# Kernel optimization log

Measured on AMD Instinct MI355X. Metric: run time of the kernel, lower is better.

Reference implementation:

```python
import jax, jax.numpy as jnp
import numpy as np

HEAD_DIM = 64
SELECT = 256  # number of selected rows/cols (m)
NUM_ITER = 4  # Newton-Schulz iterations


def _select_idx(T, mask, m):
    # top-k over sum of features (select_type='sum'), done under stop_gradient (torch.no_grad)
    somme = jax.lax.stop_gradient(jnp.sum(T, axis=-1))  # [B,H,N]
    neg = -jnp.finfo(somme.dtype).max
    somme = jnp.where(mask[:, None, :], somme, neg)
    _, idx = jax.lax.top_k(somme, m)  # [B,H,m], descending like argsort(descending=True)[:m]
    return idx


def _gather_rows(T, idx):
    # T: [B,H,N,D], idx: [B,H,m] -> [B,H,m,D]  (index_select over flattened (b h n))
    return jnp.take_along_axis(T, idx[..., None], axis=2)


def _iterative_inv(mat, num_iter):
    m = mat.shape[-1]
    I = jnp.eye(m, dtype=mat.dtype)
    K = mat
    # V0 = K^T / max_j(sum_i K_ij)
    scale = 1.0 / jnp.max(jnp.sum(K, axis=-2), axis=-1)[:, :, None, None]
    V = scale * jnp.swapaxes(K, -1, -2)
    for _ in range(num_iter):
        KV = jnp.matmul(K, V)
        V = jnp.matmul(0.25 * V, 13.0 * I - jnp.matmul(KV, 15.0 * I - jnp.matmul(KV, 7.0 * I - KV)))
    return V


def setup_inputs() -> dict:
    key = jax.random.key(0)
    kq, kk, kv = jax.random.split(key, 3)
    B, H, N, D = 2, 8, 4096, HEAD_DIM
    Q = jax.random.normal(kq, (B, H, N, D), dtype=jnp.float32)
    K = jax.random.normal(kk, (B, H, N, D), dtype=jnp.float32)
    V = jax.random.normal(kv, (B, H, N, D), dtype=jnp.float32)
    mask = jnp.ones((B, N), dtype=bool)
    return {"Q": Q, "K": K, "V": V, "mask": mask}


def reference(Q, K, V, mask):
    m = SELECT
    Qs = Q / np.sqrt(HEAD_DIM).astype(np.float32)
    # select_mode='default' -> index_select_different: indices for K from K, for Q from (scaled) Q
    idx_k = _select_idx(K, mask, m)
    idx_q = _select_idx(Qs, mask, m)
    nc = _gather_rows(K, idx_k)   # [B,H,m,D] selected columns (from K)
    nr = _gather_rows(Qs, idx_k := idx_q if False else idx_q) if False else _gather_rows(Qs, idx_q)  # [B,H,m,D]
    c = jnp.einsum('bhnd,bhmd->bhnm', Qs, nc)   # [B,H,N,m]
    r = jnp.einsum('bhmd,bhnd->bhmn', nr, K)    # [B,H,m,N]
    neg = -jnp.finfo(Qs.dtype).max
    r = jnp.where(mask[:, None, None, :], r, neg)
    kernel_1 = jax.nn.softmax(c, axis=-1)                 # [B,H,N,m]
    u = _gather_rows(kernel_1, idx_q)                     # [B,H,m,m]
    kernel_3 = jax.nn.softmax(r, axis=-1)                 # [B,H,m,N]
    kernel_2_inv = _iterative_inv(u, NUM_ITER)            # [B,H,m,m]
    RV = jnp.matmul(kernel_3, V)                          # [B,H,m,D]
    X = jnp.matmul(kernel_1, jnp.matmul(kernel_2_inv, RV))  # [B,H,N,D]
    return X
```

## Files before the change

### kernel.cpp

```cpp
#include <hip/hip_runtime.h>
#include <float.h>


#define G    16
#define NSEQ 4096
#define DH   64
#define MSEL 256
#define NSL  16

typedef __attribute__((ext_vector_type(8))) short short8;
typedef __attribute__((ext_vector_type(4))) float floatx4;
typedef __attribute__((ext_vector_type(4))) unsigned short ushort4v;
typedef unsigned short ush;

static __device__ __forceinline__ ush f2b(float x) {
    union { float f; unsigned u; } c{x};
    unsigned r = c.u + 0x7FFFu + ((c.u >> 16) & 1u);
    return (ush)(r >> 16);
}
static __device__ __forceinline__ float b2f(ush h) {
    union { unsigned u; float f; } c{(unsigned)h << 16};
    return c.f;
}
static __device__ __forceinline__ void split_store(ush* __restrict__ h, ush* __restrict__ l,
                                                   int off, float4 v, float scale) {
    float a0 = v.x * scale, a1 = v.y * scale, a2 = v.z * scale, a3 = v.w * scale;
    ush h0 = f2b(a0), h1 = f2b(a1), h2 = f2b(a2), h3 = f2b(a3);
    ushort4v hv = { h0, h1, h2, h3 };
    ushort4v lv = { f2b(a0 - b2f(h0)), f2b(a1 - b2f(h1)), f2b(a2 - b2f(h2)), f2b(a3 - b2f(h3)) };
    *(ushort4v*)&h[off] = hv;
    *(ushort4v*)&l[off] = lv;
}
static __device__ __forceinline__ floatx4 mfma3(short8 ah, short8 al, short8 bh, short8 bl, floatx4 acc) {
    acc = __builtin_amdgcn_mfma_f32_16x16x32_bf16(al, bh, acc, 0, 0, 0);
    acc = __builtin_amdgcn_mfma_f32_16x16x32_bf16(ah, bl, acc, 0, 0, 0);
    acc = __builtin_amdgcn_mfma_f32_16x16x32_bf16(ah, bh, acc, 0, 0, 0);
    return acc;
}

__global__ __launch_bounds__(256) void rowsum_kernel(const float* __restrict__ Q, const float* __restrict__ K,
                                                     float* __restrict__ sumQ, float* __restrict__ sumK,
                                                     float* __restrict__ k2) {
    long row = (long)blockIdx.x * 16 + (threadIdx.x >> 4);
    int c4 = (threadIdx.x & 15) * 4;
    float4 q = *(const float4*)(Q + row * DH + c4);
    float4 k = *(const float4*)(K + row * DH + c4);
    float qs = q.x + q.y + q.z + q.w;
    float ks = k.x + k.y + k.z + k.w;
    float k2s = k.x * k.x + k.y * k.y + k.z * k.z + k.w * k.w;
#pragma unroll
    for (int off = 8; off; off >>= 1) {
        qs += __shfl_xor(qs, off); ks += __shfl_xor(ks, off); k2s += __shfl_xor(k2s, off);
    }
    if ((threadIdx.x & 15) == 0) { sumQ[row] = qs; sumK[row] = ks; k2[row] = k2s; }
}

__global__ __launch_bounds__(256) void topk_select(const float* __restrict__ sumQ, const float* __restrict__ sumK,
                                                   int* __restrict__ idxQ, int* __restrict__ idxK,
                                                   const float* __restrict__ k2, float* __restrict__ Kmax2,
                                                   float* __restrict__ colsum) {
    __shared__ unsigned red[4];
    __shared__ float redf[4];
    __shared__ unsigned eqpre[64];
    __shared__ unsigned cnt_sel;
    int g = blockIdx.x, which = blockIdx.y;
    const float* s = (which ? sumK : sumQ) + (long)g * NSEQ;
    int* out = (which ? idxK : idxQ) + g * MSEL;
    int t = threadIdx.x, lane = t & 63, wid = t >> 6;
    if (which == 0) colsum[g * 256 + t] = 0.f;
    unsigned k[16];
#pragma unroll
    for (int i = 0; i < 16; i++) {
        unsigned u = __float_as_uint(s[t + 256 * i]);
        k[i] = (u & 0x80000000u) ? ~u : (u | 0x80000000u);
    }
    unsigned T = 0;
    for (int b = 31; b >= 0; b--) {
        unsigned trial = T | (1u << b);
        int c = 0;
#pragma unroll
        for (int i = 0; i < 16; i++) c += (k[i] >= trial);
#pragma unroll
        for (int off = 32; off; off >>= 1) c += __shfl_xor(c, off);
        __syncthreads();
        if (lane == 0) red[wid] = (unsigned)c;
        __syncthreads();
        unsigned tot = red[0] + red[1] + red[2] + red[3];
        if (tot == MSEL) { T = trial; break; }
        if (tot > MSEL) T = trial;
    }
    int cg = 0;
#pragma unroll
    for (int i = 0; i < 16; i++) cg += (k[i] > T);
#pragma unroll
    for (int off = 32; off; off >>= 1) cg += __shfl_xor(cg, off);
    __syncthreads();
    if (lane == 0) red[wid] = (unsigned)cg;
    if (t == 0) cnt_sel = 0;
    __syncthreads();
    unsigned ngreater = red[0] + red[1] + red[2] + red[3];
    unsigned want_eq = MSEL - ngreater;
#pragma unroll
    for (int i = 0; i < 16; i++) {
        unsigned long long be = __ballot(k[i] == T);
        if (lane == 0) eqpre[i * 4 + wid] = (unsigned)__popcll(be);
    }
    __syncthreads();
    if (t == 0) {
        unsigned run = 0;
        for (int j = 0; j < 64; j++) { unsigned c = eqpre[j]; eqpre[j] = run; run += c; }
    }
    __syncthreads();
#pragma unroll
    for (int i = 0; i < 16; i++) {
        int idx = t + 256 * i;
        unsigned long long lt = (1ull << lane) - 1;
        bool gt = (k[i] > T);
        unsigned long long bg = __ballot(gt);
        unsigned wbase = 0;
        if (lane == 0) wbase = atomicAdd(&cnt_sel, (unsigned)__popcll(bg));
        wbase = __shfl((int)wbase, 0);
        if (gt) out[wbase + __popcll(bg & lt)] = idx;
        bool eq = (k[i] == T);
        unsigned long long be = __ballot(eq);
        if (eq) {
            unsigned rank = eqpre[i * 4 + wid] + (unsigned)__popcll(be & lt);
            if (rank < want_eq) out[ngreater + rank] = idx;
        }
    }
    if (which == 1) {
        float mx = 0.f;
#pragma unroll
        for (int i = 0; i < 16; i++) mx = fmaxf(mx, k2[(long)g * NSEQ + t + 256 * i]);
#pragma unroll
        for (int off = 32; off; off >>= 1) mx = fmaxf(mx, __shfl_xor(mx, off));
        __syncthreads();
        if (lane == 0) redf[wid] = mx;
        __syncthreads();
        if (t == 0) Kmax2[g] = fmaxf(fmaxf(redf[0], redf[1]), fmaxf(redf[2], redf[3]));
    }
}

__global__ __launch_bounds__(256) void gather_kernel(const float* __restrict__ Q, const float* __restrict__ K,
                                                     const int* __restrict__ idxQ, const int* __restrict__ idxK,
                                                     const float* __restrict__ Kmax2,
                                                     float* __restrict__ nr,
                                                     ush* __restrict__ ncH, ush* __restrict__ ncL,
                                                     float* __restrict__ Mb) {
    int wid = threadIdx.x >> 6, lane = threadIdx.x & 63;
    long t = (long)blockIdx.x * 4 + wid;
    long g = t >> 8;
    int iq = idxQ[t], ik = idxK[t];
    float qv = Q[(g * NSEQ + iq) * DH + lane] * 0.125f;
    nr[t * DH + lane] = qv;
    float kv = K[(g * NSEQ + ik) * DH + lane];
    ush h = f2b(kv);
    ncH[t * DH + lane] = h;
    ncL[t * DH + lane] = f2b(kv - b2f(h));
    float n2 = qv * qv;
#pragma unroll
    for (int off = 32; off; off >>= 1) n2 += __shfl_xor(n2, off);
    if (lane == 0) Mb[t] = sqrtf(n2 * Kmax2[g]);
}

__global__ __launch_bounds__(256, 4) void flash_rv(const float* __restrict__ nr, const float* __restrict__ K,
                                                   const float* __restrict__ V, const float* __restrict__ Mb,
                                                   float* __restrict__ Lp, float* __restrict__ RVp) {
    __shared__ __align__(16) ush B1h[64 * 72];
    __shared__ __align__(16) ush B1l[64 * 72];
    __shared__ __align__(16) ush Ph[64 * 72];
    __shared__ float msh[64];
    __shared__ float lred[64][2];
    int ns = blockIdx.x, s = blockIdx.y, g = blockIdx.z;
    int t = threadIdx.x, lane = t & 63, w = t >> 6;
    int wr = w >> 1, wc = w & 1, ml = lane & 15, quad = lane >> 4;
    int lr = t >> 2, lq = t & 3;
    const float* nrg = nr + (long)g * 16384 + (long)s * 64 * 64;
    const float* Kg  = K + (long)g * 262144 + (long)ns * 256 * 64;
    const float* Vg  = V + (long)g * 262144 + (long)ns * 256 * 64;
    short8 Ah[2][2], Al[2][2];
#pragma unroll
    for (int i2 = 0; i2 < 2; i2++)
#pragma unroll
        for (int kq = 0; kq < 2; kq++) {
            const float* p = nrg + (wr * 32 + i2 * 16 + ml) * 64 + kq * 32 + quad * 8;
            float4 f0 = *(const float4*)p;
            float4 f1 = *(const float4*)(p + 4);
            float vals[8] = { f0.x, f0.y, f0.z, f0.w, f1.x, f1.y, f1.z, f1.w };
            short8 hh, ll;
#pragma unroll
            for (int j = 0; j < 8; j++) {
                ush h = f2b(vals[j]);
                hh[j] = (short)h;
                ll[j] = (short)f2b(vals[j] - b2f(h));
            }
            Ah[i2][kq] = hh; Al[i2][kq] = ll;
        }
    if (t < 64) msh[t] = Mb[g * 256 + s * 64 + t];
    float lsum[2][4] = {};
    floatx4 acc[2][2] = {};
    int vn = t >> 2, vdq = (t & 3) * 16;
    for (int it = 0; it < 4; it++) {
        __syncthreads();
        float4 kv[4], vv[4];
#pragma unroll
        for (int q = 0; q < 4; q++) kv[q] = *(const float4*)(Kg + (long)(it * 64 + lr) * 64 + lq * 16 + q * 4);
#pragma unroll
        for (int q = 0; q < 4; q++) vv[q] = *(const float4*)(Vg + (long)(it * 64 + vn) * 64 + vdq + q * 4);
#pragma unroll
        for (int q = 0; q < 4; q++) split_store(B1h, B1l, lr * 72 + lq * 16 + q * 4, kv[q], 1.0f);
        __syncthreads();
        floatx4 sa[2][2] = {};
#pragma unroll
        for (int kq = 0; kq < 2; kq++) {
            short8 b0h = *(const short8*)&B1h[(wc * 32 + ml) * 72 + kq * 32 + quad * 8];
            short8 b0l = *(const short8*)&B1l[(wc * 32 + ml) * 72 + kq * 32 + quad * 8];
            short8 b1h = *(const short8*)&B1h[(wc * 32 + 16 + ml) * 72 + kq * 32 + quad * 8];
            short8 b1l = *(const short8*)&B1l[(wc * 32 + 16 + ml) * 72 + kq * 32 + quad * 8];
            sa[0][0] = mfma3(Ah[0][kq], Al[0][kq], b0h, b0l, sa[0][0]);
            sa[0][1] = mfma3(Ah[0][kq], Al[0][kq], b1h, b1l, sa[0][1]);
            sa[1][0] = mfma3(Ah[1][kq], Al[1][kq], b0h, b0l, sa[1][0]);
            sa[1][1] = mfma3(Ah[1][kq], Al[1][kq], b1h, b1l, sa[1][1]);
        }
        __syncthreads();
#pragma unroll
        for (int i2 = 0; i2 < 2; i2++)
#pragma unroll
            for (int r = 0; r < 4; r++) {
                int row = wr * 32 + i2 * 16 + quad * 4 + r;
                float M = msh[row];
                float p0 = __expf(sa[i2][0][r] - M);
                float p1 = __expf(sa[i2][1][r] - M);
                lsum[i2][r] += p0 + p1;
                Ph[row * 72 + wc * 32 + ml] = f2b(p0);
                Ph[row * 72 + wc * 32 + 16 + ml] = f2b(p1);
            }
#pragma unroll
        for (int q = 0; q < 4; q++)
#pragma unroll
            for (int c = 0; c < 4; c++) {
                int d = vdq + q * 4 + c;
                int addr = d * 72 + ((((vn >> 3) ^ ((d >> 4) & 3)) << 3) | (vn & 7));
                B1h[addr] = f2b((&vv[q].x)[c]);
            }
        __syncthreads();
#pragma unroll
        for (int kq = 0; kq < 2; kq++) {
            short8 a0 = *(const short8*)&Ph[(wr * 32 + ml) * 72 + kq * 32 + quad * 8];
            short8 a1 = *(const short8*)&Ph[(wr * 32 + 16 + ml) * 72 + kq * 32 + quad * 8];
            int nb = kq * 4 + quad;
            short8 b0 = *(const short8*)&B1h[(wc * 32 + ml) * 72 + ((nb ^ (2 * wc)) << 3)];
            short8 b1 = *(const short8*)&B1h[(wc * 32 + 16 + ml) * 72 + ((nb ^ (2 * wc + 1)) << 3)];
            acc[0][0] = __builtin_amdgcn_mfma_f32_16x16x32_bf16(a0, b0, acc[0][0], 0, 0, 0);
            acc[0][1] = __builtin_amdgcn_mfma_f32_16x16x32_bf16(a0, b1, acc[0][1], 0, 0, 0);
            acc[1][0] = __builtin_amdgcn_mfma_f32_16x16x32_bf16(a1, b0, acc[1][0], 0, 0, 0);
            acc[1][1] = __builtin_amdgcn_mfma_f32_16x16x32_bf16(a1, b1, acc[1][1], 0, 0, 0);
        }
    }
#pragma unroll
    for (int i2 = 0; i2 < 2; i2++)
#pragma unroll
        for (int r = 0; r < 4; r++) {
            float v = lsum[i2][r];
#pragma unroll
            for (int off = 8; off; off >>= 1) v += __shfl_xor(v, off);
            if (ml == 0) lred[wr * 32 + i2 * 16 + quad * 4 + r][wc] = v;
        }
    __syncthreads();
    long p = ((long)(g * 4 + s)) * NSL + ns;
    if (t < 64) Lp[p * 64 + t] = lred[t][0] + lred[t][1];
    float* rvp = RVp + p * 4096;
#pragma unroll
    for (int i2 = 0; i2 < 2; i2++)
#pragma unroll
        for (int j2 = 0; j2 < 2; j2++)
#pragma unroll
            for (int r = 0; r < 4; r++)
                rvp[(wr * 32 + i2 * 16 + quad * 4 + r) * 64 + wc * 32 + j2 * 16 + ml] = acc[i2][j2][r];
}

__global__ __launch_bounds__(256) void rv_merge(const float* __restrict__ Lp, const float* __restrict__ RVp,
                                                ush* __restrict__ RVt) {
    int g = blockIdx.y;
    int s = blockIdx.x >> 2, mq = blockIdx.x & 3;
    int t = threadIdx.x;
    int d = t & 63;
    int m0 = mq * 16 + (t >> 6) * 4;
    long pb = ((long)(g * 4 + s)) * NSL;
#pragma unroll
    for (int mm = 0; mm < 4; mm++) {
        int rho = m0 + mm;
        float L = 0.f, val = 0.f;
#pragma unroll
        for (int n = 0; n < NSL; n++) {
            L   += Lp[(pb + n) * 64 + rho];
            val += RVp[(pb + n) * 4096 + rho * 64 + d];
        }
        RVt[(long)g * 16384 + d * 256 + s * 64 + rho] = f2b(val / L);
    }
}

template <int MODE>
__global__ __launch_bounds__(256, 4) void fused_cx(const float* __restrict__ A,
                                                   const ush* __restrict__ ncH, const ush* __restrict__ ncL,
                                                   const ush* __restrict__ WtH, const ush* __restrict__ WtL,
                                                   float* __restrict__ Out, float* __restrict__ colsum,
                                                   float ascale) {
    __shared__ __align__(16) ush SM[18432];
    ush* Ah = SM;            ush* Al = SM + 4608;
    ush* Bh = SM + 9216;     ush* Bl = SM + 13824;
    ush* Ph = SM;            ush* Pl = SM + 4608;
    ush* Wh = SM + 9216;     ush* Wl = SM + 13824;
    __shared__ float pm[256], ps[256], Mr[64], Lr[64];
    int strip = blockIdx.x, g = blockIdx.y;
    int t = threadIdx.x, lane = t & 63, w = t >> 6;
    int wr = w >> 1, wc = w & 1, ml = lane & 15, quad = lane >> 4;
    int lr = t >> 2, lq = t & 3;
    long aRows = (MODE == 0) ? 4096 : 256;
    const float* Ag = A + (long)g * aRows * 64 + (long)strip * 64 * 64;
    const ush* ncHg = ncH + (long)g * 16384;
    const ush* ncLg = ncL + (long)g * 16384;
#pragma unroll
    for (int q = 0; q < 4; q++) {
        float4 v = *(const float4*)(Ag + lr * 64 + lq * 16 + q * 4);
        split_store(Ah, Al, lr * 72 + lq * 16 + q * 4, v, ascale);
    }
    floatx4 sacc[4][4] = {};
    for (int c = 0; c < 4; c++) {
        __syncthreads();
        {
            const ush* sH = ncHg + (c * 64 + lr) * 64;
            const ush* sL = ncLg + (c * 64 + lr) * 64;
            *(uint4*)&Bh[lr * 72 + lq * 8]       = *(const uint4*)&sH[lq * 8];
            *(uint4*)&Bh[lr * 72 + (lq + 4) * 8] = *(const uint4*)&sH[(lq + 4) * 8];
            *(uint4*)&Bl[lr * 72 + lq * 8]       = *(const uint4*)&sL[lq * 8];
            *(uint4*)&Bl[lr * 72 + (lq + 4) * 8] = *(const uint4*)&sL[(lq + 4) * 8];
        }
        __syncthreads();
#pragma unroll
        for (int kq = 0; kq < 2; kq++) {
            short8 bh = *(const short8*)&Bh[(w * 16 + ml) * 72 + kq * 32 + quad * 8];
            short8 bl = *(const short8*)&Bl[(w * 16 + ml) * 72 + kq * 32 + quad * 8];
#pragma unroll
            for (int i = 0; i < 4; i++) {
                short8 afh = *(const short8*)&Ah[(16 * i + ml) * 72 + kq * 32 + quad * 8];
                short8 afl = *(const short8*)&Al[(16 * i + ml) * 72 + kq * 32 + quad * 8];
                sacc[c][i] = mfma3(afh, afl, bh, bl, sacc[c][i]);
            }
        }
    }
#pragma unroll
    for (int i = 0; i < 4; i++)
#pragma unroll
        for (int r = 0; r < 4; r++) {
            float mx = fmaxf(fmaxf(sacc[0][i][r], sacc[1][i][r]), fmaxf(sacc[2][i][r], sacc[3][i][r]));
#pragma unroll
            for (int off = 8; off; off >>= 1) mx = fmaxf(mx, __shfl_xor(mx, off));
            if (ml == 0) pm[(16 * i + quad * 4 + r) * 4 + w] = mx;
        }
    __syncthreads();
    if (t < 64) Mr[t] = fmaxf(fmaxf(pm[t * 4], pm[t * 4 + 1]), fmaxf(pm[t * 4 + 2], pm[t * 4 + 3]));
    __syncthreads();
#pragma unroll
    for (int i = 0; i < 4; i++)
#pragma unroll
        for (int r = 0; r < 4; r++) {
            int row = 16 * i + quad * 4 + r;
            float M = Mr[row];
            float sum = 0.f;
#pragma unroll
            for (int c = 0; c < 4; c++) {
                float p = __expf(sacc[c][i][r] - M);
                sacc[c][i][r] = p;
                sum += p;
            }
#pragma unroll
            for (int off = 8; off; off >>= 1) sum += __shfl_xor(sum, off);
            if (ml == 0) ps[row * 4 + w] = sum;
        }
    __syncthreads();
    if (t < 64) Lr[t] = ps[t * 4] + ps[t * 4 + 1] + ps[t * 4 + 2] + ps[t * 4 + 3];
    __syncthreads();
    if (MODE == 1) {
        float invL[4][4];
#pragma unroll
        for (int i = 0; i < 4; i++)
#pragma unroll
            for (int r = 0; r < 4; r++) invL[i][r] = 1.0f / Lr[16 * i + quad * 4 + r];
        float* ug = Out + (long)g * 65536 + (long)strip * 64 * 256;
#pragma unroll
        for (int i = 0; i < 4; i++)
#pragma unroll
            for (int r = 0; r < 4; r++) {
                int row = 16 * i + quad * 4 + r;
#pragma unroll
                for (int c = 0; c < 4; c++)
                    ug[(long)row * 256 + c * 64 + w * 16 + ml] = sacc[c][i][r] * invL[i][r];
            }
#pragma unroll
        for (int c = 0; c < 4; c++) {
            float v = 0.f;
#pragma unroll
            for (int i = 0; i < 4; i++)
#pragma unroll
                for (int r = 0; r < 4; r++) v += sacc[c][i][r] * invL[i][r];
            v += __shfl_xor(v, 16);
            v += __shfl_xor(v, 32);
            if (quad == 0) atomicAdd(&colsum[g * 256 + c * 64 + w * 16 + ml], v);
        }
        return;
    }
    floatx4 xacc[2][2] = {};
    const ush* wHg = WtH + (long)g * 16384;
    const ush* wLg = WtL + (long)g * 16384;
#pragma unroll
    for (int h = 0; h < 4; h++) {
        __syncthreads();
#pragma unroll
        for (int i = 0; i < 4; i++)
#pragma unroll
            for (int r = 0; r < 4; r++) {
                int row = 16 * i + quad * 4 + r;
                float p = sacc[h][i][r];
                ush hh = f2b(p);
                Ph[row * 72 + w * 16 + ml] = hh;
                Pl[row * 72 + w * 16 + ml] = f2b(p - b2f(hh));
            }
        {
            const ush* sH = wHg + lr * 256 + h * 64;
            const ush* sL = wLg + lr * 256 + h * 64;
            *(uint4*)&Wh[lr * 72 + lq * 8]       = *(const uint4*)&sH[lq * 8];
            *(uint4*)&Wh[lr * 72 + (lq + 4) * 8] = *(const uint4*)&sH[(lq + 4) * 8];
            *(uint4*)&Wl[lr * 72 + lq * 8]       = *(const uint4*)&sL[lq * 8];
            *(uint4*)&Wl[lr * 72 + (lq + 4) * 8] = *(const uint4*)&sL[(lq + 4) * 8];
        }
        __syncthreads();
#pragma unroll
        for (int kq = 0; kq < 2; kq++) {
            short8 a0h = *(const short8*)&Ph[(wr * 32 + ml) * 72 + kq * 32 + quad * 8];
            short8 a0l = *(const short8*)&Pl[(wr * 32 + ml) * 72 + kq * 32 + quad * 8];
            short8 a1h = *(const short8*)&Ph[(wr * 32 + 16 + ml) * 72 + kq * 32 + quad * 8];
            short8 a1l = *(const short8*)&Pl[(wr * 32 + 16 + ml) * 72 + kq * 32 + quad * 8];
            short8 b0h = *(const short8*)&Wh[(wc * 32 + ml) * 72 + kq * 32 + quad * 8];
            short8 b0l = *(const short8*)&Wl[(wc * 32 + ml) * 72 + kq * 32 + quad * 8];
            short8 b1h = *(const short8*)&Wh[(wc * 32 + 16 + ml) * 72 + kq * 32 + quad * 8];
            short8 b1l = *(const short8*)&Wl[(wc * 32 + 16 + ml) * 72 + kq * 32 + quad * 8];
            xacc[0][0] = mfma3(a0h, a0l, b0h, b0l, xacc[0][0]);
            xacc[0][1] = mfma3(a0h, a0l, b1h, b1l, xacc[0][1]);
            xacc[1][0] = mfma3(a1h, a1l, b0h, b0l, xacc[1][0]);
            xacc[1][1] = mfma3(a1h, a1l, b1h, b1l, xacc[1][1]);
        }
    }
    float* outg = Out + (long)g * 262144 + (long)strip * 64 * 64;
#pragma unroll
    for (int i2 = 0; i2 < 2; i2++)
#pragma unroll
        for (int j2 = 0; j2 < 2; j2++)
#pragma unroll
            for (int r = 0; r < 4; r++) {
                int row = wr * 32 + i2 * 16 + quad * 4 + r;
                outg[(long)row * 64 + wc * 32 + j2 * 16 + ml] = xacc[i2][j2][r] / Lr[row];
            }
}

__global__ __launch_bounds__(256) void ns_prep_kernel(const float* __restrict__ u, const float* __restrict__ colsum,
                                                      ush* __restrict__ u_bf, ush* __restrict__ V0,
                                                      float* __restrict__ scale) {
    __shared__ float tile[64][65];
    __shared__ float smax[4];
    int g = blockIdx.z, tr = blockIdx.y, tc = blockIdx.x;
    int t = threadIdx.x, lane = t & 63, wid = t >> 6;
    float v = colsum[g * 256 + t];
#pragma unroll
    for (int off = 32; off; off >>= 1) v = fmaxf(v, __shfl_xor(v, off));
    if (lane == 0) smax[wid] = v;
    __syncthreads();
    float sc = 1.0f / fmaxf(fmaxf(smax[0], smax[1]), fmaxf(smax[2], smax[3]));
    if (t == 0 && tr == 0 && tc == 0) scale[g] = sc;
    long base = (long)g * MSEL * MSEL;
    const float* ug = u + base;
    int cq = (t & 15) * 4, r0 = t >> 4;
#pragma unroll
    for (int i = 0; i < 4; i++) {
        int r = r0 + 16 * i;
        float4 vv = *(const float4*)&ug[(long)(tr * 64 + r) * MSEL + tc * 64 + cq];
        long o = base + (long)(tr * 64 + r) * MSEL + tc * 64 + cq;
        ushort4v ub = { f2b(vv.x), f2b(vv.y), f2b(vv.z), f2b(vv.w) };
        *(ushort4v*)&u_bf[o] = ub;
        tile[r][cq] = vv.x; tile[r][cq + 1] = vv.y; tile[r][cq + 2] = vv.z; tile[r][cq + 3] = vv.w;
    }
    __syncthreads();
#pragma unroll
    for (int i = 0; i < 4; i++) {
        int r = r0 + 16 * i;
        ushort4v o = { f2b(sc * tile[cq][r]), f2b(sc * tile[cq + 1][r]),
                       f2b(sc * tile[cq + 2][r]), f2b(sc * tile[cq + 3][r]) };
        *(ushort4v*)&V0[base + (long)(tc * 64 + r) * MSEL + tr * 64 + cq] = o;
    }
}

template <int MODE>
__global__ __launch_bounds__(256) void ns2(const ush* __restrict__ A0, const ush* __restrict__ A1,
                                           const ush* __restrict__ Bt,
                                           ush* __restrict__ O0rm, ush* __restrict__ O0t,
                                           ush* __restrict__ O1rm, ush* __restrict__ O1t,
                                           const ush* __restrict__ Et_in, const ush* __restrict__ St_in,
                                           const float* __restrict__ scale) {
    const int LD = 136;
    __shared__ __align__(16) ush As[64 * LD];
    __shared__ __align__(16) ush Bs[64 * LD];
    int z = blockIdx.z, g = z & 15, which = z >> 4;
    int tm = blockIdx.y, tn = blockIdx.x;
    long base = (long)g * 65536;
    const ush* A = which ? A1 : A0;
    ush* Orm = which ? O1rm : O0rm;
    ush* Ot  = which ? O1t  : O0t;
    const ush* Ag = A + base + (long)tm * 64 * 256;
    long bbase = (MODE >= 3) ? (long)g * 16384 : base;
    const ush* Bg = Bt + bbase + (long)tn * 64 * 256;
    int t = threadIdx.x;
    int lr = t >> 2, lq = t & 3;
    int w = t >> 6, lane = t & 63;
    int wr = w >> 1, wc = w & 1;
    int ml = lane & 15, quad = lane >> 4;
    floatx4 acc[2][2] = {};
#pragma unroll
    for (int h = 0; h < 2; h++) {
        __syncthreads();
#pragma unroll
        for (int rr = 0; rr < 4; rr++) {
            int col = (lq + 4 * rr) * 8;
            *(uint4*)&As[lr * LD + col] = *(const uint4*)(Ag + lr * 256 + h * 128 + col);
            *(uint4*)&Bs[lr * LD + col] = *(const uint4*)(Bg + lr * 256 + h * 128 + col);
        }
        __syncthreads();
#pragma unroll
        for (int kq = 0; kq < 4; kq++) {
            int ko = kq * 32 + quad * 8;
            short8 a0 = *(const short8*)&As[(wr * 32 + ml) * LD + ko];
            short8 a1 = *(const short8*)&As[(wr * 32 + 16 + ml) * LD + ko];
            short8 b0 = *(const short8*)&Bs[(wc * 32 + ml) * LD + ko];
            short8 b1 = *(const short8*)&Bs[(wc * 32 + 16 + ml) * LD + ko];
            acc[0][0] = __builtin_amdgcn_mfma_f32_16x16x32_bf16(a0, b0, acc[0][0], 0, 0, 0);
            acc[0][1] = __builtin_amdgcn_mfma_f32_16x16x32_bf16(a0, b1, acc[0][1], 0, 0, 0);
            acc[1][0] = __builtin_amdgcn_mfma_f32_16x16x32_bf16(a1, b0, acc[1][0], 0, 0, 0);
            acc[1][1] = __builtin_amdgcn_mfma_f32_16x16x32_bf16(a1, b1, acc[1][1], 0, 0, 0);
        }
    }
    float sc = (MODE == 1) ? scale[g] : 1.0f;
    int rowb = tm * 64 + wr * 32, colb = tn * 64 + wc * 32;
#pragma unroll
    for (int i = 0; i < 2; i++) {
#pragma unroll
        for (int j = 0; j < 2; j++) {
            int col = colb + j * 16 + ml;
            int r0 = rowb + i * 16 + quad * 4;
            float v[4];
#pragma unroll
            for (int r = 0; r < 4; r++) v[r] = acc[i][j][r];
            if (MODE == 1) {
#pragma unroll
                for (int r = 0; r < 4; r++) v[r] *= sc;
            } else if (MODE == 2) {
                ushort4v et = *(const ushort4v*)&Et_in[base + (long)col * 256 + r0];
                ushort4v st = *(const ushort4v*)&St_in[base + (long)col * 256 + r0];
#pragma unroll
                for (int r = 0; r < 4; r++)
                    v[r] = 0.25f * (((r0 + r == col) ? 13.0f : 0.0f)
                                    - 15.0f * b2f(et[r]) + 7.0f * b2f(st[r]) - v[r]);
            }
            if (MODE == 3) {
                ushort4v ht = { f2b(v[0]), f2b(v[1]), f2b(v[2]), f2b(v[3]) };
                *(ushort4v*)&Ot[(long)g * 16384 + (long)col * 256 + r0] = ht;
            } else if (MODE == 4) {
                ushort4v hv, lv;
#pragma unroll
                for (int r = 0; r < 4; r++) {
                    ush h = f2b(v[r]);
                    hv[r] = h;
                    lv[r] = f2b(v[r] - b2f(h));
                }
                *(ushort4v*)&O0rm[(long)g * 16384 + (long)col * 256 + r0] = hv;
                *(ushort4v*)&O0t[(long)g * 16384 + (long)col * 256 + r0] = lv;
            } else {
                ush h[4];
#pragma unroll
                for (int r = 0; r < 4; r++) h[r] = f2b(v[r]);
#pragma unroll
                for (int r = 0; r < 4; r++) Orm[base + (long)(r0 + r) * 256 + col] = h[r];
                ushort4v ht = { h[0], h[1], h[2], h[3] };
                *(ushort4v*)&Ot[base + (long)col * 256 + r0] = ht;
            }
        }
    }
}

extern "C" void kernel_launch(void* const* d_in, const int* in_sizes, int n_in,
                              void* d_out, int out_size, void* d_ws, size_t ws_size,
                              hipStream_t stream) {
    (void)in_sizes; (void)n_in; (void)out_size; (void)ws_size;
    const float* Q = (const float*)d_in[0];
    const float* K = (const float*)d_in[1];
    const float* V = (const float*)d_in[2];

    float* ws    = (float*)d_ws;
    float* sumQ  = ws;
    float* sumK  = sumQ + 65536;
    float* k2    = sumK + 65536;
    float* nr    = k2 + 65536;
    float* u     = nr + 262144;
    float* Mb    = u + 1048576;
    float* Kmax2 = Mb + 4096;
    float* scale = Kmax2 + 16;
    float* colsum= scale + 16 + 32;
    float* Lp    = colsum + 4096;
    float* RVp   = Lp + 65536;
    int* idxQ    = (int*)(RVp + 4194304);
    int* idxK    = idxQ + 4096;
    ush* ncH     = (ush*)(idxK + 4096);
    ush* ncL     = ncH + 262144;
    ush* WtH     = ncL + 262144;
    ush* WtL     = WtH + 262144;
    ush* RVt     = WtL + 262144;
    ush* PRt     = RVt + 262144;
    ush* u_bf    = PRt + 262144;
    ush* Vacc_a  = u_bf + 1048576;
    ush* Vacc_b  = Vacc_a + 1048576;
    ush* VaccTj  = Vacc_b + 1048576;
    ush* E_a     = VaccTj + 1048576;
    ush* Et_a    = E_a + 1048576;
    ush* E_b     = Et_a + 1048576;
    ush* Et_b    = E_b + 1048576;
    ush* Sbuf    = Et_b + 1048576;
    ush* St      = Sbuf + 1048576;
    ush* Pbuf    = St + 1048576;
    ush* Pt      = Pbuf + 1048576;

    dim3 blk(256);

    hipLaunchKernelGGL(rowsum_kernel, dim3(G * NSEQ / 16), blk, 0, stream, Q, K, sumQ, sumK, k2);
    hipLaunchKernelGGL(topk_select, dim3(G, 2), blk, 0, stream, sumQ, sumK, idxQ, idxK, k2, Kmax2, colsum);
    hipLaunchKernelGGL(gather_kernel, dim3(G * MSEL / 4), blk, 0, stream, Q, K, idxQ, idxK, Kmax2, nr, ncH, ncL, Mb);

    hipLaunchKernelGGL(flash_rv, dim3(NSL, 4, G), blk, 0, stream, nr, K, V, Mb, Lp, RVp);
    hipLaunchKernelGGL(rv_merge, dim3(16, G), blk, 0, stream, Lp, RVp, RVt);

    hipLaunchKernelGGL((fused_cx<1>), dim3(4, G), blk, 0, stream, nr, ncH, ncL,
                       (const ush*)0, (const ush*)0, u, colsum, 1.0f);

    hipLaunchKernelGGL(ns_prep_kernel, dim3(4, 4, G), blk, 0, stream, u, colsum, u_bf, Vacc_a, scale);

    hipLaunchKernelGGL((ns2<1>), dim3(4, 4, G), blk, 0, stream,
                       u_bf, (const ush*)0, u_bf, E_a, Et_a, (ush*)0, (ush*)0,
                       (const ush*)0, (const ush*)0, scale);

    ush* E = E_a;  ush* Et = Et_a;
    ush* En = E_b; ush* Ent = Et_b;
    ush* Vc = Vacc_a; ush* Vn = Vacc_b;
    for (int i = 0; i < 4; i++) {
        hipLaunchKernelGGL((ns2<0>), dim3(4, 4, G), blk, 0, stream,
                           E, (const ush*)0, Et, Sbuf, St, (ush*)0, (ush*)0,
                           (const ush*)0, (const ush*)0, (const float*)0);
        hipLaunchKernelGGL((ns2<2>), dim3(4, 4, G), blk, 0, stream,
                           Sbuf, (const ush*)0, Et, Pbuf, Pt, (ush*)0, (ush*)0,
                           Et, St, (const float*)0);
        if (i < 3) {
            hipLaunchKernelGGL((ns2<0>), dim3(4, 4, 2 * G), blk, 0, stream,
                               E, Vc, Pt, En, Ent, Vn, VaccTj,
                               (const ush*)0, (const ush*)0, (const float*)0);
            ush* tp;
            tp = E; E = En; En = tp;
            tp = Et; Et = Ent; Ent = tp;
            tp = Vc; Vc = Vn; Vn = tp;
        }
    }
    hipLaunchKernelGGL((ns2<3>), dim3(1, 4, G), blk, 0, stream,
                       Pbuf, (const ush*)0, RVt, (ush*)0, PRt, (ush*)0, (ush*)0,
                       (const ush*)0, (const ush*)0, (const float*)0);
    hipLaunchKernelGGL((ns2<4>), dim3(1, 4, G), blk, 0, stream,
                       Vc, (const ush*)0, PRt, WtH, WtL, (ush*)0, (ush*)0,
                       (const ush*)0, (const ush*)0, (const float*)0);

    hipLaunchKernelGGL((fused_cx<0>), dim3(64, G), blk, 0, stream, Q, ncH, ncL, WtH, WtL,
                       (float*)d_out, (float*)0, 0.125f);
}
```

Measured before the change: 262.4 us.

## Restructure Newton-Schulz inverse chain into fused dual-GEMM steps and merge prep kernels

Rewrites the iterative inverse schedule. The next E = K·V is computed algebraically inside the step kernel from E, S=E², and E³, so the separate E² GEMM per iteration disappears. Each nsB block now computes two products, E³ and E⁴, and writes both P and the next E. The final P·RV ordering becomes V·P then (·RV), and rv_merge is folded into the ns prep kernel, which cuts launches. The risk is extra bf16 error accumulation, because E is now derived from polynomial terms instead of a direct product.

```diff
diff --git a/kernel.cpp b/kernel.cpp
--- a/kernel.cpp
+++ b/kernel.cpp
@@ -277,27 +277,6 @@
 #pragma unroll
             for (int r = 0; r < 4; r++)
                 rvp[(wr * 32 + i2 * 16 + quad * 4 + r) * 64 + wc * 32 + j2 * 16 + ml] = acc[i2][j2][r];
-}
-
-__global__ __launch_bounds__(256) void rv_merge(const float* __restrict__ Lp, const float* __restrict__ RVp,
-                                                ush* __restrict__ RVt) {
-    int g = blockIdx.y;
-    int s = blockIdx.x >> 2, mq = blockIdx.x & 3;
-    int t = threadIdx.x;
-    int d = t & 63;
-    int m0 = mq * 16 + (t >> 6) * 4;
-    long pb = ((long)(g * 4 + s)) * NSL;
-#pragma unroll
-    for (int mm = 0; mm < 4; mm++) {
-        int rho = m0 + mm;
-        float L = 0.f, val = 0.f;
-#pragma unroll
-        for (int n = 0; n < NSL; n++) {
-            L   += Lp[(pb + n) * 64 + rho];
-            val += RVp[(pb + n) * 4096 + rho * 64 + d];
-        }
-        RVt[(long)g * 16384 + d * 256 + s * 64 + rho] = f2b(val / L);
-    }
 }
 
 template <int MODE>
@@ -463,13 +442,34 @@
             }
 }
 
-__global__ __launch_bounds__(256) void ns_prep_kernel(const float* __restrict__ u, const float* __restrict__ colsum,
-                                                      ush* __restrict__ u_bf, ush* __restrict__ V0,
-                                                      float* __restrict__ scale) {
+__global__ __launch_bounds__(256) void mergeprep_kernel(const float* __restrict__ Lp, const float* __restrict__ RVp,
+                                                        ush* __restrict__ RVt,
+                                                        const float* __restrict__ u, const float* __restrict__ colsum,
+                                                        ush* __restrict__ u_bf, ush* __restrict__ V0,
+                                                        float* __restrict__ scale) {
     __shared__ float tile[64][65];
     __shared__ float smax[4];
-    int g = blockIdx.z, tr = blockIdx.y, tc = blockIdx.x;
+    int g = blockIdx.y;
     int t = threadIdx.x, lane = t & 63, wid = t >> 6;
+    if (blockIdx.z == 0) {
+        int s = blockIdx.x >> 2, mq = blockIdx.x & 3;
+        int d = t & 63;
+        int m0 = mq * 16 + (t >> 6) * 4;
+        long pb = ((long)(g * 4 + s)) * NSL;
+#pragma unroll
+        for (int mm = 0; mm < 4; mm++) {
+            int rho = m0 + mm;
+            float L = 0.f, val = 0.f;
+#pragma unroll
+            for (int n = 0; n < NSL; n++) {
+                L   += Lp[(pb + n) * 64 + rho];
+                val += RVp[(pb + n) * 4096 + rho * 64 + d];
+            }
+            RVt[(long)g * 16384 + d * 256 + s * 64 + rho] = f2b(val / L);
+        }
+        return;
+    }
+    int tc = blockIdx.x & 3, tr = (blockIdx.x >> 2) & 3;
     float v = colsum[g * 256 + t];
 #pragma unroll
     for (int off = 32; off; off >>= 1) v = fmaxf(v, __shfl_xor(v, off));
@@ -499,25 +499,19 @@
     }
 }
 
-template <int MODE>
-__global__ __launch_bounds__(256) void ns2(const ush* __restrict__ A0, const ush* __restrict__ A1,
-                                           const ush* __restrict__ Bt,
-                                           ush* __restrict__ O0rm, ush* __restrict__ O0t,
-                                           ush* __restrict__ O1rm, ush* __restrict__ O1t,
-                                           const ush* __restrict__ Et_in, const ush* __restrict__ St_in,
-                                           const float* __restrict__ scale) {
+__global__ __launch_bounds__(256) void nsAC(const ush* __restrict__ A0, const ush* __restrict__ B0t,
+                                            const ush* __restrict__ A1, const ush* __restrict__ B1t,
+                                            ush* __restrict__ C0rm, ush* __restrict__ C0t,
+                                            ush* __restrict__ C1rm,
+                                            const float* __restrict__ scale, int whichBase) {
     const int LD = 136;
     __shared__ __align__(16) ush As[64 * LD];
     __shared__ __align__(16) ush Bs[64 * LD];
-    int z = blockIdx.z, g = z & 15, which = z >> 4;
+    int z = blockIdx.z, g = z & 15, which = (z >> 4) + whichBase;
     int tm = blockIdx.y, tn = blockIdx.x;
     long base = (long)g * 65536;
-    const ush* A = which ? A1 : A0;
-    ush* Orm = which ? O1rm : O0rm;
-    ush* Ot  = which ? O1t  : O0t;
-    const ush* Ag = A + base + (long)tm * 64 * 256;
-    long bbase = (MODE >= 3) ? (long)g * 16384 : base;
-    const ush* Bg = Bt + bbase + (long)tn * 64 * 256;
+    const ush* Ag = (which ? A1 : A0) + base + (long)tm * 64 * 256;
+    const ush* Bg = (which ? B1t : B0t) + base + (long)tn * 64 * 256;
     int t = threadIdx.x;
     int lr = t >> 2, lq = t & 3;
     int w = t >> 6, lane = t & 63;
@@ -547,7 +541,7 @@
             acc[1][1] = __builtin_amdgcn_mfma_f32_16x16x32_bf16(a1, b1, acc[1][1], 0, 0, 0);
         }
     }
-    float sc = (MODE == 1) ? scale[g] : 1.0f;
+    float sc = (which == 0 && scale) ? scale[g] : 1.0f;
     int rowb = tm * 64 + wr * 32, colb = tn * 64 + wc * 32;
 #pragma unroll
     for (int i = 0; i < 2; i++) {
@@ -555,42 +549,164 @@
         for (int j = 0; j < 2; j++) {
             int col = colb + j * 16 + ml;
             int r0 = rowb + i * 16 + quad * 4;
-            float v[4];
-#pragma unroll
-            for (int r = 0; r < 4; r++) v[r] = acc[i][j][r];
-            if (MODE == 1) {
-#pragma unroll
-                for (int r = 0; r < 4; r++) v[r] *= sc;
-            } else if (MODE == 2) {
-                ushort4v et = *(const ushort4v*)&Et_in[base + (long)col * 256 + r0];
-                ushort4v st = *(const ushort4v*)&St_in[base + (long)col * 256 + r0];
-#pragma unroll
-                for (int r = 0; r < 4; r++)
-                    v[r] = 0.25f * (((r0 + r == col) ? 13.0f : 0.0f)
-                                    - 15.0f * b2f(et[r]) + 7.0f * b2f(st[r]) - v[r]);
-            }
-            if (MODE == 3) {
-                ushort4v ht = { f2b(v[0]), f2b(v[1]), f2b(v[2]), f2b(v[3]) };
-                *(ushort4v*)&Ot[(long)g * 16384 + (long)col * 256 + r0] = ht;
-            } else if (MODE == 4) {
-                ushort4v hv, lv;
+            ush h[4];
+#pragma unroll
+            for (int r = 0; r < 4; r++) h[r] = f2b(acc[i][j][r] * sc);
+            if (which == 0) {
+#pragma unroll
+                for (int r = 0; r < 4; r++) C0rm[base + (long)(r0 + r) * 256 + col] = h[r];
+                ushort4v ht = { h[0], h[1], h[2], h[3] };
+                *(ushort4v*)&C0t[base + (long)col * 256 + r0] = ht;
+            } else {
+#pragma unroll
+                for (int r = 0; r < 4; r++) C1rm[base + (long)(r0 + r) * 256 + col] = h[r];
+            }
+        }
+    }
+}
+
+template <bool FINAL>
+__global__ __launch_bounds__(256) void nsB(const ush* __restrict__ S, const ush* __restrict__ Et,
+                                           const ush* __restrict__ St,
+                                           ush* __restrict__ Eo, ush* __restrict__ Eot,
+                                           ush* __restrict__ Pt) {
+    const int LD = 136;
+    __shared__ __align__(16) ush As[64 * LD];
+    __shared__ __align__(16) ush B1s[64 * LD];
+    __shared__ __align__(16) ush B2s[64 * LD];
+    int g = blockIdx.z, tm = blockIdx.y, tn = blockIdx.x;
+    long base = (long)g * 65536;
+    const ush* Ag  = S + base + (long)tm * 64 * 256;
+    const ush* B1g = Et + base + (long)tn * 64 * 256;
+    const ush* B2g = St + base + (long)tn * 64 * 256;
+    int t = threadIdx.x;
+    int lr = t >> 2, lq = t & 3;
+    int w = t >> 6, lane = t & 63;
+    int wr = w >> 1, wc = w & 1;
+    int ml = lane & 15, quad = lane >> 4;
+    floatx4 acc1[2][2] = {};
+    floatx4 acc2[2][2] = {};
+#pragma unroll
+    for (int h = 0; h < 2; h++) {
+        __syncthreads();
+#pragma unroll
+        for (int rr = 0; rr < 4; rr++) {
+            int col = (lq + 4 * rr) * 8;
+            *(uint4*)&As[lr * LD + col]  = *(const uint4*)(Ag + lr * 256 + h * 128 + col);
+            *(uint4*)&B1s[lr * LD + col] = *(const uint4*)(B1g + lr * 256 + h * 128 + col);
+            if (!FINAL) *(uint4*)&B2s[lr * LD + col] = *(const uint4*)(B2g + lr * 256 + h * 128 + col);
+        }
+        __syncthreads();
+#pragma unroll
+        for (int kq = 0; kq < 4; kq++) {
+            int ko = kq * 32 + quad * 8;
+            short8 a0 = *(const short8*)&As[(wr * 32 + ml) * LD + ko];
+            short8 a1 = *(const short8*)&As[(wr * 32 + 16 + ml) * LD + ko];
+            short8 b10 = *(const short8*)&B1s[(wc * 32 + ml) * LD + ko];
+            short8 b11 = *(const short8*)&B1s[(wc * 32 + 16 + ml) * LD + ko];
+            acc1[0][0] = __builtin_amdgcn_mfma_f32_16x16x32_bf16(a0, b10, acc1[0][0], 0, 0, 0);
+            acc1[0][1] = __builtin_amdgcn_mfma_f32_16x16x32_bf16(a0, b11, acc1[0][1], 0, 0, 0);
+            acc1[1][0] = __builtin_amdgcn_mfma_f32_16x16x32_bf16(a1, b10, acc1[1][0], 0, 0, 0);
+            acc1[1][1] = __builtin_amdgcn_mfma_f32_16x16x32_bf16(a1, b11, acc1[1][1], 0, 0, 0);
+            if (!FINAL) {
+                short8 b20 = *(const short8*)&B2s[(wc * 32 + ml) * LD + ko];
+                short8 b21 = *(const short8*)&B2s[(wc * 32 + 16 + ml) * LD + ko];
+                acc2[0][0] = __builtin_amdgcn_mfma_f32_16x16x32_bf16(a0, b20, acc2[0][0], 0, 0, 0);
+                acc2[0][1] = __builtin_amdgcn_mfma_f32_16x16x32_bf16(a0, b21, acc2[0][1], 0, 0, 0);
+                acc2[1][0] = __builtin_amdgcn_mfma_f32_16x16x32_bf16(a1, b20, acc2[1][0], 0, 0, 0);
+                acc2[1][1] = __builtin_amdgcn_mfma_f32_16x16x32_bf16(a1, b21, acc2[1][1], 0, 0, 0);
+            }
+        }
+    }
+    int rowb = tm * 64 + wr * 32, colb = tn * 64 + wc * 32;
+#pragma unroll
+    for (int i = 0; i < 2; i++) {
+#pragma unroll
+        for (int j = 0; j < 2; j++) {
+            int col = colb + j * 16 + ml;
+            int r0 = rowb + i * 16 + quad * 4;
+            ushort4v et = *(const ushort4v*)&Et[base + (long)col * 256 + r0];
+            ushort4v st = *(const ushort4v*)&St[base + (long)col * 256 + r0];
+            ushort4v pv;
+#pragma unroll
+            for (int r = 0; r < 4; r++) {
+                float e = b2f(et[r]), s = b2f(st[r]);
+                float p = 0.25f * (((r0 + r == col) ? 13.0f : 0.0f) - 15.0f * e + 7.0f * s - acc1[i][j][r]);
+                pv[r] = f2b(p);
+            }
+            *(ushort4v*)&Pt[base + (long)col * 256 + r0] = pv;
+            if (!FINAL) {
+                ush h[4];
 #pragma unroll
                 for (int r = 0; r < 4; r++) {
-                    ush h = f2b(v[r]);
-                    hv[r] = h;
-                    lv[r] = f2b(v[r] - b2f(h));
+                    float e = b2f(et[r]), s = b2f(st[r]);
+                    float en = 0.25f * (13.0f * e - 15.0f * s + 7.0f * acc1[i][j][r] - acc2[i][j][r]);
+                    h[r] = f2b(en);
                 }
-                *(ushort4v*)&O0rm[(long)g * 16384 + (long)col * 256 + r0] = hv;
-                *(ushort4v*)&O0t[(long)g * 16384 + (long)col * 256 + r0] = lv;
-            } else {
-                ush h[4];
-#pragma unroll
-                for (int r = 0; r < 4; r++) h[r] = f2b(v[r]);
-#pragma unroll
-                for (int r = 0; r < 4; r++) Orm[base + (long)(r0 + r) * 256 + col] = h[r];
+#pragma unroll
+                for (int r = 0; r < 4; r++) Eo[base + (long)(r0 + r) * 256 + col] = h[r];
                 ushort4v ht = { h[0], h[1], h[2], h[3] };
-                *(ushort4v*)&Ot[base + (long)col * 256 + r0] = ht;
-            }
+                *(ushort4v*)&Eot[base + (long)col * 256 + r0] = ht;
+            }
+        }
+    }
+}
+
+__global__ __launch_bounds__(256) void nsW(const ush* __restrict__ V4, const ush* __restrict__ RVt,
+                                           ush* __restrict__ WtH, ush* __restrict__ WtL) {
+    const int LD = 136;
+    __shared__ __align__(16) ush As[64 * LD];
+    __shared__ __align__(16) ush Bs[64 * LD];
+    int g = blockIdx.z, tm = blockIdx.y;
+    long base = (long)g * 65536;
+    const ush* Ag = V4 + base + (long)tm * 64 * 256;
+    const ush* Bg = RVt + (long)g * 16384;
+    int t = threadIdx.x;
+    int lr = t >> 2, lq = t & 3;
+    int w = t >> 6, lane = t & 63;
+    int wr = w >> 1, wc = w & 1;
+    int ml = lane & 15, quad = lane >> 4;
+    floatx4 acc[2][2] = {};
+#pragma unroll
+    for (int h = 0; h < 2; h++) {
+        __syncthreads();
+#pragma unroll
+        for (int rr = 0; rr < 4; rr++) {
+            int col = (lq + 4 * rr) * 8;
+            *(uint4*)&As[lr * LD + col] = *(const uint4*)(Ag + lr * 256 + h * 128 + col);
+            *(uint4*)&Bs[lr * LD + col] = *(const uint4*)(Bg + lr * 256 + h * 128 + col);
+        }
+        __syncthreads();
+#pragma unroll
+        for (int kq = 0; kq < 4; kq++) {
+            int ko = kq * 32 + quad * 8;
+            short8 a0 = *(const short8*)&As[(wr * 32 + ml) * LD + ko];
+            short8 a1 = *(const short8*)&As[(wr * 32 + 16 + ml) * LD + ko];
+            short8 b0 = *(const short8*)&Bs[(wc * 32 + ml) * LD + ko];
+            short8 b1 = *(const short8*)&Bs[(wc * 32 + 16 + ml) * LD + ko];
+            acc[0][0] = __builtin_amdgcn_mfma_f32_16x16x32_bf16(a0, b0, acc[0][0], 0, 0, 0);
+            acc[0][1] = __builtin_amdgcn_mfma_f32_16x16x32_bf16(a0, b1, acc[0][1], 0, 0, 0);
+            acc[1][0] = __builtin_amdgcn_mfma_f32_16x16x32_bf16(a1, b0, acc[1][0], 0, 0, 0);
+            acc[1][1] = __builtin_amdgcn_mfma_f32_16x16x32_bf16(a1, b1, acc[1][1], 0, 0, 0);
+        }
+    }
+    int rowb = tm * 64 + wr * 32, colb = wc * 32;
+#pragma unroll
+    for (int i = 0; i < 2; i++) {
+#pragma unroll
+        for (int j = 0; j < 2; j++) {
+            int col = colb + j * 16 + ml;
+            int r0 = rowb + i * 16 + quad * 4;
+            ushort4v hv, lv;
+#pragma unroll
+            for (int r = 0; r < 4; r++) {
+                float v = acc[i][j][r];
+                ush h = f2b(v);
+                hv[r] = h;
+                lv[r] = f2b(v - b2f(h));
+            }
+            *(ushort4v*)&WtH[(long)g * 16384 + (long)col * 256 + r0] = hv;
+            *(ushort4v*)&WtL[(long)g * 16384 + (long)col * 256 + r0] = lv;
         }
     }
 }
@@ -622,19 +738,16 @@
     ush* WtH     = ncL + 262144;
     ush* WtL     = WtH + 262144;
     ush* RVt     = WtL + 262144;
-    ush* PRt     = RVt + 262144;
-    ush* u_bf    = PRt + 262144;
+    ush* u_bf    = RVt + 262144;
     ush* Vacc_a  = u_bf + 1048576;
     ush* Vacc_b  = Vacc_a + 1048576;
-    ush* VaccTj  = Vacc_b + 1048576;
-    ush* E_a     = VaccTj + 1048576;
+    ush* E_a     = Vacc_b + 1048576;
     ush* Et_a    = E_a + 1048576;
     ush* E_b     = Et_a + 1048576;
     ush* Et_b    = E_b + 1048576;
     ush* Sbuf    = Et_b + 1048576;
     ush* St      = Sbuf + 1048576;
-    ush* Pbuf    = St + 1048576;
-    ush* Pt      = Pbuf + 1048576;
+    ush* Ptb     = St + 1048576;
 
     dim3 blk(256);
 
@@ -643,43 +756,34 @@
     hipLaunchKernelGGL(gather_kernel, dim3(G * MSEL / 4), blk, 0, stream, Q, K, idxQ, idxK, Kmax2, nr, ncH, ncL, Mb);
 
     hipLaunchKernelGGL(flash_rv, dim3(NSL, 4, G), blk, 0, stream, nr, K, V, Mb, Lp, RVp);
-    hipLaunchKernelGGL(rv_merge, dim3(16, G), blk, 0, stream, Lp, RVp, RVt);
 
     hipLaunchKernelGGL((fused_cx<1>), dim3(4, G), blk, 0, stream, nr, ncH, ncL,
                        (const ush*)0, (const ush*)0, u, colsum, 1.0f);
 
-    hipLaunchKernelGGL(ns_prep_kernel, dim3(4, 4, G), blk, 0, stream, u, colsum, u_bf, Vacc_a, scale);
-
-    hipLaunchKernelGGL((ns2<1>), dim3(4, 4, G), blk, 0, stream,
-                       u_bf, (const ush*)0, u_bf, E_a, Et_a, (ush*)0, (ush*)0,
-                       (const ush*)0, (const ush*)0, scale);
+    hipLaunchKernelGGL(mergeprep_kernel, dim3(16, G, 2), blk, 0, stream,
+                       Lp, RVp, RVt, u, colsum, u_bf, Vacc_a, scale);
+
+    hipLaunchKernelGGL(nsAC, dim3(4, 4, G), blk, 0, stream,
+                       u_bf, u_bf, (const ush*)0, (const ush*)0, E_a, Et_a, (ush*)0, scale, 0);
+    hipLaunchKernelGGL(nsAC, dim3(4, 4, G), blk, 0, stream,
+                       E_a, Et_a, (const ush*)0, (const ush*)0, Sbuf, St, (ush*)0, (const float*)0, 0);
 
     ush* E = E_a;  ush* Et = Et_a;
     ush* En = E_b; ush* Ent = Et_b;
     ush* Vc = Vacc_a; ush* Vn = Vacc_b;
-    for (int i = 0; i < 4; i++) {
-        hipLaunchKernelGGL((ns2<0>), dim3(4, 4, G), blk, 0, stream,
-                           E, (const ush*)0, Et, Sbuf, St, (ush*)0, (ush*)0,
-                           (const ush*)0, (const ush*)0, (const float*)0);
-        hipLaunchKernelGGL((ns2<2>), dim3(4, 4, G), blk, 0, stream,
-                           Sbuf, (const ush*)0, Et, Pbuf, Pt, (ush*)0, (ush*)0,
-                           Et, St, (const float*)0);
-        if (i < 3) {
-            hipLaunchKernelGGL((ns2<0>), dim3(4, 4, 2 * G), blk, 0, stream,
-                               E, Vc, Pt, En, Ent, Vn, VaccTj,
-                               (const ush*)0, (const ush*)0, (const float*)0);
-            ush* tp;
-            tp = E; E = En; En = tp;
-            tp = Et; Et = Ent; Ent = tp;
-            tp = Vc; Vc = Vn; Vn = tp;
-        }
-    }
-    hipLaunchKernelGGL((ns2<3>), dim3(1, 4, G), blk, 0, stream,
-                       Pbuf, (const ush*)0, RVt, (ush*)0, PRt, (ush*)0, (ush*)0,
-                       (const ush*)0, (const ush*)0, (const float*)0);
-    hipLaunchKernelGGL((ns2<4>), dim3(1, 4, G), blk, 0, stream,
-                       Vc, (const ush*)0, PRt, WtH, WtL, (ush*)0, (ush*)0,
-                       (const ush*)0, (const ush*)0, (const float*)0);
+    for (int i = 0; i < 3; i++) {
+        hipLaunchKernelGGL((nsB<false>), dim3(4, 4, G), blk, 0, stream, Sbuf, Et, St, En, Ent, Ptb);
+        hipLaunchKernelGGL(nsAC, dim3(4, 4, 2 * G), blk, 0, stream,
+                           En, Ent, Vc, Ptb, Sbuf, St, Vn, (const float*)0, 0);
+        ush* tp;
+        tp = E; E = En; En = tp;
+        tp = Et; Et = Ent; Ent = tp;
+        tp = Vc; Vc = Vn; Vn = tp;
+    }
+    hipLaunchKernelGGL((nsB<true>), dim3(4, 4, G), blk, 0, stream, Sbuf, Et, St, (ush*)0, (ush*)0, Ptb);
+    hipLaunchKernelGGL(nsAC, dim3(4, 4, G), blk, 0, stream,
+                       (const ush*)0, (const ush*)0, Vc, Ptb, (ush*)0, (ush*)0, Vn, (const float*)0, 1);
+    hipLaunchKernelGGL(nsW, dim3(1, 4, G), blk, 0, stream, Vn, RVt, WtH, WtL);
 
     hipLaunchKernelGGL((fused_cx<0>), dim3(64, G), blk, 0, stream, Q, ncH, ncL, WtH, WtL,
                        (float*)d_out, (float*)0, 0.125f);
```

Result: faster. 255.3 us (median of 2 runs) (-2.7%).
